# Kernel tuning notes

Hardware: AMD Instinct MI355X
Metric: run time of the kernel (lower is better)

The kernel has to match this reference:

```python
import jax, jax.numpy as jnp
import numpy as np

HEADS = 8
DIM_HEAD = 64
NB_FEATURES = 256
CHUNK = 128          # chunk size used by performer's causal_linear_attention_noncuda
EPS_KERNEL = 1e-4    # eps in softmax_kernel feature map
EPS_DENOM = 1e-6     # eps added to k_cumsum in the denominator


def softmax_kernel(data, proj, is_query):
    # FAVOR+ positive softmax random features (performer_pytorch.softmax_kernel)
    # data: [B,H,N,D], proj: [M,D]
    d = data.shape[-1]
    normalizer = d ** -0.25
    ratio = proj.shape[0] ** -0.5
    data_dash = jnp.einsum('bhnd,md->bhnm', data * normalizer, proj)
    # ||x||^2 / (2*sqrt(d))
    diag = jnp.sum(data * data, axis=-1, keepdims=True) * 0.5 * (normalizer ** 2)
    if is_query:
        m = jax.lax.stop_gradient(jnp.max(data_dash, axis=-1, keepdims=True))
    else:
        m = jax.lax.stop_gradient(jnp.max(data_dash, axis=(-1, -2), keepdims=True))
    return ratio * (jnp.exp(data_dash - diag - m) + EPS_KERNEL)


def causal_linear_attention(qp, kp, v, chunk=CHUNK):
    # Chunked causal linear attention (O(N) in seq len):
    # out_i = q'_i . S_i / (q'_i . z_i), S_i = sum_{j<=i} k'_j v_j^T, z_i = cumsum k'_j
    B, H, N, M = qp.shape
    E = v.shape[-1]
    C = N // chunk

    def to_chunks(x):
        return x.reshape(B, H, C, chunk, x.shape[-1]).transpose(2, 0, 1, 3, 4)

    qc, kc, vc = to_chunks(qp), to_chunks(kp), to_chunks(v)
    k0 = jnp.zeros((B, H, M), qp.dtype)
    s0 = jnp.zeros((B, H, M, E), qp.dtype)

    def step(carry, inp):
        k_last, s_last = carry
        q, k, vv = inp  # [B,H,c,M], [B,H,c,M], [B,H,c,E]
        k_cum = k_last[:, :, None, :] + jnp.cumsum(k, axis=2)           # [B,H,c,M]
        d_inv = 1.0 / jnp.einsum('bhnm,bhnm->bhn', q, k_cum + EPS_DENOM)
        ctx = jnp.einsum('bhnm,bhne->bhnme', k, vv)                      # [B,H,c,M,E]
        s_cum = s_last[:, :, None] + jnp.cumsum(ctx, axis=2)             # [B,H,c,M,E]
        out = jnp.einsum('bhnme,bhnm,bhn->bhne', s_cum, q, d_inv)        # [B,H,c,E]
        return (k_cum[:, :, -1, :], s_cum[:, :, -1]), out

    _, outs = jax.lax.scan(step, (k0, s0), (qc, kc, vc))  # [C,B,H,c,E]
    return outs.transpose(1, 2, 0, 3, 4).reshape(B, H, N, E)


def setup_inputs() -> dict:
    key = jax.random.key(0)
    k1, k2, k3, k4 = jax.random.split(key, 4)
    B, N, D = 4, 2048, 512
    return {
        'query': jax.random.normal(k1, (B, N, D), jnp.float32),
        'key': jax.random.normal(k2, (B, N, D), jnp.float32),
        'value': jax.random.normal(k3, (B, N, D), jnp.float32),
        'projection': jax.random.normal(k4, (NB_FEATURES, DIM_HEAD), jnp.float32),
    }


def reference(query, key, value, projection):
    B, N, D = query.shape

    def split(x):  # [B,N,D] -> [B,H,N,Dh]
        return x.reshape(B, N, HEADS, DIM_HEAD).transpose(0, 2, 1, 3)

    q, k, v = split(query), split(key), split(value)
    qp = softmax_kernel(q, projection, is_query=True)
    kp = softmax_kernel(k, projection, is_query=False)
    out = causal_linear_attention(qp, kp, v)
    return out.transpose(0, 2, 1, 3).reshape(B, N, D)
```

## Files before the change

### kernel.cpp

```cpp
#include <hip/hip_runtime.h>
#include <math.h>

#define BB 4
#define NN 2048
#define DD 512
#define HH 8
#define DH 64
#define MM 256
#define BH 32
#define CHK 128
#define NCH 16
#define ROWS (BH*NN)

constexpr float NRM   = 0.35355339059327373f;
constexpr float RATIO = 0.0625f;
constexpr float EPSK  = 1e-4f;
constexpr float EPSD  = 1e-6f;
constexpr float REPS  = 0.0625f * 1e-4f;

#define OFFB_QP   ((size_t)0)
#define OFFB_SP   ((size_t)33554432)
#define OFFB_KP   (OFFB_SP + (size_t)16777216)
#define OFFB_VT   (OFFB_KP + (size_t)33554432)
#define OFFB_Z    (OFFB_VT + (size_t)8388608)
#define OFFB_KMP  (OFFB_Z  + (size_t)524288)
#define OFFB_SF   (OFFB_KMP + (size_t)4096)
#define OFFB_PJB  (OFFB_SF + (size_t)4096)

typedef __attribute__((ext_vector_type(8))) short short8;
typedef __attribute__((ext_vector_type(4))) float f32x4;

__device__ __forceinline__ float b2f(ushort u) {
  union { float f; unsigned int i; } x; x.i = ((unsigned int)u) << 16; return x.f;
}
__device__ __forceinline__ ushort f2b(float f) {
  unsigned int u = __float_as_uint(f);
  unsigned int r = (u + 0x7FFFu + ((u >> 16) & 1u)) >> 16;
  return (ushort)r;
}

#define MFMA(a,b,c) __builtin_amdgcn_mfma_f32_16x16x32_bf16(a, b, c, 0, 0, 0)

__global__ __launch_bounds__(256) void prep_kernel(const float* __restrict__ proj,
                                                   char* __restrict__ ws) {
  const int i = blockIdx.x*256 + threadIdx.x;
  float4 v = *(const float4*)(proj + (size_t)i*4);
  ushort4 o;
  o.x = f2b(v.x); o.y = f2b(v.y); o.z = f2b(v.z); o.w = f2b(v.w);
  *(ushort4*)((ushort*)(ws + OFFB_PJB) + (size_t)i*4) = o;
}

template<int MODE>
__device__ __forceinline__ void featm_body(const float* __restrict__ inp,
                                           const ushort* __restrict__ projb,
                                           char* __restrict__ ws,
                                           char* lds, int blk) {
  ushort* xh = (ushort*)lds;
  ushort* xl = xh + 64*72;
  ushort* ps = xl + 64*72;
  ushort* qt = (ushort*)lds;
  float* diag_s = (float*)(lds + 36864);
  float (*wmax)[4] = (float(*)[4])(lds + 37120);
  float* kred = (float*)(lds + 38144);

  const int t  = threadIdx.x;
  const int w  = t >> 6;
  const int l  = t & 63;
  const int lq = l >> 4;
  const int ln = l & 15;

  const int rowbase = blk * 64;
  const int bh = rowbase >> 11;
  const int b  = bh >> 3, h = bh & 7;
  const int n0 = rowbase & (NN - 1);

  {
    const int r  = t >> 2;
    const int c0 = (t & 3) * 16;
    const float* src = inp + ((size_t)(b*NN + n0 + r))*DD + h*DH + c0;
    float vv[16];
    #pragma unroll
    for (int j = 0; j < 4; ++j) {
      float4 v = *(const float4*)(src + j*4);
      vv[4*j+0] = v.x*NRM; vv[4*j+1] = v.y*NRM;
      vv[4*j+2] = v.z*NRM; vv[4*j+3] = v.w*NRM;
    }
    float s = 0.f;
    ushort hi[16], lo[16];
    #pragma unroll
    for (int j = 0; j < 16; ++j) {
      s += vv[j]*vv[j];
      hi[j] = f2b(vv[j]);
      lo[j] = f2b(vv[j] - b2f(hi[j]));
    }
    *(short8*)(xh + r*72 + c0)     = *(short8*)&hi[0];
    *(short8*)(xh + r*72 + c0 + 8) = *(short8*)&hi[8];
    *(short8*)(xl + r*72 + c0)     = *(short8*)&lo[0];
    *(short8*)(xl + r*72 + c0 + 8) = *(short8*)&lo[8];
    s += __shfl_xor(s, 1); s += __shfl_xor(s, 2);
    if ((t & 3) == 0) diag_s[r] = 0.5f * s;
  }

  f32x4 acc[4][4];
  #pragma unroll
  for (int mt = 0; mt < 4; ++mt)
    #pragma unroll
    for (int c = 0; c < 4; ++c) acc[mt][c] = (f32x4){0.f,0.f,0.f,0.f};

  #pragma unroll
  for (int p = 0; p < 2; ++p) {
    if (p) __syncthreads();
    #pragma unroll
    for (int ld = 0; ld < 4; ++ld) {
      int flat = t + 256*ld;
      int r = flat >> 3, g = flat & 7;
      *(short8*)(ps + r*72 + g*8) = *(const short8*)(projb + (size_t)(p*128 + r)*DH + g*8);
    }
    __syncthreads();
    #pragma unroll
    for (int kk = 0; kk < 2; ++kk) {
      short8 ah[4], al[4];
      #pragma unroll
      for (int mt = 0; mt < 4; ++mt) {
        ah[mt] = *(const short8*)(xh + (mt*16 + ln)*72 + kk*32 + lq*8);
        al[mt] = *(const short8*)(xl + (mt*16 + ln)*72 + kk*32 + lq*8);
      }
      #pragma unroll
      for (int ntl = 0; ntl < 2; ++ntl) {
        short8 bf = *(const short8*)(ps + (w*32 + ntl*16 + ln)*72 + kk*32 + lq*8);
        #pragma unroll
        for (int mt = 0; mt < 4; ++mt) {
          acc[mt][2*p+ntl] = MFMA(al[mt], bf, acc[mt][2*p+ntl]);
          acc[mt][2*p+ntl] = MFMA(ah[mt], bf, acc[mt][2*p+ntl]);
        }
      }
    }
  }

  if (MODE == 0) {
    #pragma unroll
    for (int mt = 0; mt < 4; ++mt)
      #pragma unroll
      for (int reg = 0; reg < 4; ++reg) {
        float m = acc[mt][0][reg];
        #pragma unroll
        for (int c = 1; c < 4; ++c) m = fmaxf(m, acc[mt][c][reg]);
        m = fmaxf(m, __shfl_xor(m, 1));
        m = fmaxf(m, __shfl_xor(m, 2));
        m = fmaxf(m, __shfl_xor(m, 4));
        m = fmaxf(m, __shfl_xor(m, 8));
        if (ln == 0) wmax[mt*16 + lq*4 + reg][w] = m;
      }
  } else {
    float mx = -1e30f;
    #pragma unroll
    for (int mt = 0; mt < 4; ++mt)
      #pragma unroll
      for (int c = 0; c < 4; ++c)
        #pragma unroll
        for (int reg = 0; reg < 4; ++reg) mx = fmaxf(mx, acc[mt][c][reg]);
    #pragma unroll
    for (int m = 1; m < 64; m <<= 1) mx = fmaxf(mx, __shfl_xor(mx, m));
    if (l == 0) kred[w] = mx;
  }
  __syncthreads();

  float km = 0.f;
  if (MODE == 1) {
    km = fmaxf(fmaxf(kred[0], kred[1]), fmaxf(kred[2], kred[3]));
    if (t == 0) ((float*)(ws + OFFB_KMP))[blk] = km;
  }

  #pragma unroll
  for (int mt = 0; mt < 4; ++mt)
    #pragma unroll
    for (int reg = 0; reg < 4; ++reg) {
      const int row = mt*16 + lq*4 + reg;
      float rm;
      if (MODE == 0) {
        float4 wm4 = *(const float4*)&wmax[row][0];
        rm = fmaxf(fmaxf(wm4.x, wm4.y), fmaxf(wm4.z, wm4.w));
      } else {
        rm = km;
      }
      const float dg = diag_s[row];
      #pragma unroll
      for (int c = 0; c < 4; ++c) {
        const int f = (c >> 1)*128 + w*32 + (c & 1)*16 + ln;
        const float e = __expf(acc[mt][c][reg] - dg - rm);
        qt[row*264 + f] = f2b(MODE == 0 ? RATIO*(e + EPSK) : e);
      }
    }
  __syncthreads();

  ushort* dstbase = (ushort*)(ws + (MODE == 0 ? OFFB_QP : OFFB_KP)) + (size_t)rowbase*MM;
  #pragma unroll
  for (int ld = 0; ld < 8; ++ld) {
    int flat = t + 256*ld;
    int row = flat >> 5, g = flat & 31;
    *(short8*)(dstbase + (size_t)row*MM + g*8) = *(const short8*)(qt + row*264 + g*8);
  }
}

__device__ __forceinline__ void vt_body(const float* __restrict__ value,
                                        char* __restrict__ ws,
                                        char* lds, int blk) {
  float (*vsh)[68] = (float(*)[68])lds;
  const int t = threadIdx.x;
  const int bh = blk >> 4, nc = blk & 15;
  const int b = bh >> 3, h = bh & 7;
  const int n0 = nc * CHK;
  #pragma unroll
  for (int l = 0; l < 8; ++l) {
    int flat = t + 256*l;
    int r = flat >> 4, g = flat & 15;
    *(float4*)&vsh[r][g*4] = *(const float4*)(value + ((size_t)(b*NN + n0 + r))*DD + h*DH + g*4);
  }
  __syncthreads();
  const int e = t & 63, qd = t >> 6;
  ushort* vt = (ushort*)(ws + OFFB_VT) + ((size_t)bh*DH + e)*NN + n0 + qd*32;
  #pragma unroll
  for (int p = 0; p < 16; ++p) {
    unsigned int lo = f2b(vsh[qd*32 + 2*p][e]);
    unsigned int hi = f2b(vsh[qd*32 + 2*p + 1][e]);
    ((unsigned int*)vt)[p] = lo | (hi << 16);
  }
}

__global__ __launch_bounds__(256) void mega_kernel(const float* __restrict__ q,
                                                   const float* __restrict__ k,
                                                   const float* __restrict__ v,
                                                   char* __restrict__ ws) {
  __shared__ __align__(16) char lds[38160];
  const ushort* projb = (const ushort*)(ws + OFFB_PJB);
  const int blk = blockIdx.x;
  if (blk < 1024)       featm_body<0>(q, projb, ws, lds, blk);
  else if (blk < 2048)  featm_body<1>(k, projb, ws, lds, blk - 1024);
  else                  vt_body(v, ws, lds, blk - 2048);
}

__global__ __launch_bounds__(256) void sfac_kernel(char* __restrict__ ws) {
  const int blk = blockIdx.x*256 + threadIdx.x;
  const int bh = blk >> 5;
  const float* kmp = (const float*)(ws + OFFB_KMP);
  float km = -1e30f;
  #pragma unroll
  for (int i = 0; i < 32; ++i) km = fmaxf(km, kmp[bh*32 + i]);
  ((float*)(ws + OFFB_SF))[blk] = RATIO * __expf(kmp[blk] - km);
}

__global__ __launch_bounds__(256) void sprefix_kernel(char* __restrict__ ws) {
  __shared__ __align__(16) unsigned int kpTu[16*68];
  __shared__ __align__(16) ushort Vts[64*136];
  __shared__ float zred[16][16];

  const int t  = threadIdx.x;
  const int w  = t >> 6;
  const int l  = t & 63;
  const int lq = l >> 4;
  const int ln = l & 15;
  const int bh = blockIdx.x >> 4;
  const int ms = blockIdx.x & 15;

  const ushort* kpb = (const ushort*)(ws + OFFB_KP) + (size_t)bh*NN*MM + ms*16;
  const ushort* vtb = (const ushort*)(ws + OFFB_VT) + (size_t)bh*DH*NN;
  const float*  sf  = (const float*)(ws + OFFB_SF);
  ushort* spb = (ushort*)(ws + OFFB_SP) + (size_t)bh*NCH*DH*MM + ms*16;
  float*  zb  = (float*)(ws + OFFB_Z) + (size_t)bh*NCH*MM + ms*16;

  f32x4 acc = (f32x4){0.f,0.f,0.f,0.f};
  float zrun = 0.f;

  for (int tc = 0; tc < NCH; ++tc) {
    __syncthreads();

    if (t < 16) {
      if (tc > 0) {
        float s = 0.f;
        #pragma unroll
        for (int q = 0; q < 16; ++q) s += zred[q][t];
        zrun += s;
      }
      zb[(size_t)tc*MM + t] = zrun;
    }
    {
      ushort* sp = spb + (size_t)tc*DH*MM;
      #pragma unroll
      for (int reg = 0; reg < 4; ++reg)
        sp[(size_t)(w*16 + lq*4 + reg)*MM + ln] = f2b(acc[reg]);
    }

    const ushort* kslice = kpb + (size_t)tc*CHK*MM;
    if (t < 128) {
      int jp = t >> 1, mo = t & 1;
      float s0 = sf[bh*32 + tc*2 + (jp >> 5)];
      short8 a = *(const short8*)(kslice + (size_t)(2*jp)*MM + mo*8);
      short8 c = *(const short8*)(kslice + (size_t)(2*jp+1)*MM + mo*8);
      #pragma unroll
      for (int i = 0; i < 8; ++i) {
        ushort ua = f2b(fmaf(b2f((ushort)a[i]), s0, REPS));
        ushort uc = f2b(fmaf(b2f((ushort)c[i]), s0, REPS));
        kpTu[(mo*8 + i)*68 + jp] = (unsigned int)ua | ((unsigned int)uc << 16);
      }
    }
    #pragma unroll
    for (int it = 0; it < 4; ++it) {
      int slot = t + 256*it;
      int e = slot >> 4, g = slot & 15;
      *(short8*)(Vts + e*136 + g*8) = *(const short8*)(vtb + (size_t)e*NN + tc*CHK + g*8);
    }
    __syncthreads();

    {
      int m = t & 15, q = t >> 4;
      float s = 0.f;
      #pragma unroll
      for (int u = 0; u < 4; ++u) {
        unsigned int p = kpTu[m*68 + q*4 + u];
        s += b2f((ushort)(p & 0xFFFF)) + b2f((ushort)(p >> 16));
      }
      zred[q][m] = s;
    }

    #pragma unroll
    for (int kk = 0; kk < 4; ++kk) {
      short8 af = *(const short8*)(Vts + (w*16 + ln)*136 + kk*32 + lq*8);
      short8 bf = *(const short8*)((const ushort*)kpTu + (size_t)ln*136 + kk*32 + lq*8);
      acc = MFMA(af, bf, acc);
    }
  }
}

__global__ __launch_bounds__(256) void fused_kernel(float* __restrict__ out,
                                                    char* __restrict__ ws) {
  __shared__ __align__(16) char lds[52224];
  __shared__ float den_i[128];
  __shared__ float dinv_s[128];

  const int t  = threadIdx.x;
  const int w  = t >> 6;
  const int l  = t & 63;
  const int lq = l >> 4;
  const int ln = l & 15;
  const int rt0 = w;
  const int rt1 = 7 - w;
  const int blk = blockIdx.x;
  const int bh = blk >> 4, tc = blk & 15;
  const int b = bh >> 3, h = bh & 7;
  const size_t rowbase = (size_t)bh*NN + tc*CHK;

  const ushort* qpg = (const ushort*)(ws + OFFB_QP) + rowbase*MM;
  const ushort* kpg = (const ushort*)(ws + OFFB_KP) + rowbase*MM;
  const ushort* spg = (const ushort*)(ws + OFFB_SP) + (size_t)blk*DH*MM;
  const float*  sf  = (const float*)(ws + OFFB_SF);
  const float sc0 = sf[blk*2], sc1 = sf[blk*2 + 1];

  ushort* qs = (ushort*)lds;
  ushort* ks = qs + 128*72;
  ushort* ss = ks + 128*72;

  f32x4 acc[2][8];
  #pragma unroll
  for (int mt = 0; mt < 2; ++mt)
    #pragma unroll
    for (int nt = 0; nt < 8; ++nt) acc[mt][nt] = (f32x4){0.f,0.f,0.f,0.f};
  f32x4 oacc[2][4];
  #pragma unroll
  for (int mt = 0; mt < 2; ++mt)
    #pragma unroll
    for (int nt = 0; nt < 4; ++nt) oacc[mt][nt] = (f32x4){0.f,0.f,0.f,0.f};

  for (int mc = 0; mc < 4; ++mc) {
    __syncthreads();
    #pragma unroll
    for (int ld2 = 0; ld2 < 4; ++ld2) {
      int flat = t + 256*ld2; int r = flat >> 3, g = flat & 7;
      *(short8*)(qs + r*72 + g*8) = *(const short8*)(qpg + (size_t)r*MM + mc*64 + g*8);
    }
    #pragma unroll
    for (int ld2 = 0; ld2 < 4; ++ld2) {
      int flat = t + 256*ld2; int r = flat >> 3, g = flat & 7;
      short8 kv = *(const short8*)(kpg + (size_t)r*MM + mc*64 + g*8);
      const float sc = (r & 64) ? sc1 : sc0;
      ushort ov[8];
      #pragma unroll
      for (int i = 0; i < 8; ++i) ov[i] = f2b(fmaf(b2f((ushort)kv[i]), sc, REPS));
      *(short8*)(ks + r*72 + g*8) = *(short8*)&ov[0];
    }
    #pragma unroll
    for (int ld2 = 0; ld2 < 2; ++ld2) {
      int flat = t + 256*ld2; int e = flat >> 3, g = flat & 7;
      *(short8*)(ss + e*72 + g*8) = *(const short8*)(spg + (size_t)e*MM + mc*64 + g*8);
    }
    __syncthreads();
    #pragma unroll
    for (int kk = 0; kk < 2; ++kk) {
      short8 af0 = *(const short8*)(qs + (rt0*16 + ln)*72 + kk*32 + lq*8);
      short8 af1 = *(const short8*)(qs + (rt1*16 + ln)*72 + kk*32 + lq*8);
      #pragma unroll
      for (int nt = 0; nt < 8; ++nt) {
        if (nt <= rt1) {
          short8 bf = *(const short8*)(ks + (nt*16 + ln)*72 + kk*32 + lq*8);
          if (nt <= rt0) acc[0][nt] = MFMA(af0, bf, acc[0][nt]);
          acc[1][nt] = MFMA(af1, bf, acc[1][nt]);
        }
      }
      #pragma unroll
      for (int nt = 0; nt < 4; ++nt) {
        short8 bf = *(const short8*)(ss + (nt*16 + ln)*72 + kk*32 + lq*8);
        oacc[0][nt] = MFMA(af0, bf, oacc[0][nt]);
        oacc[1][nt] = MFMA(af1, bf, oacc[1][nt]);
      }
    }
  }

  __syncthreads();

  ushort* P   = (ushort*)lds;
  ushort* Vts = (ushort*)(lds + 34816);

  float rs[2][4] = {{0,0,0,0},{0,0,0,0}};
  #pragma unroll
  for (int mt = 0; mt < 2; ++mt) {
    const int ibase = (mt ? rt1 : rt0) * 16;
    #pragma unroll
    for (int nt = 0; nt < 8; ++nt)
      #pragma unroll
      for (int reg = 0; reg < 4; ++reg) {
        int i = ibase + lq*4 + reg;
        int j = nt*16 + ln;
        float v = (j <= i) ? acc[mt][nt][reg] : 0.f;
        rs[mt][reg] += v;
        P[i*136 + j] = f2b(v);
      }
  }
  #pragma unroll
  for (int mt = 0; mt < 2; ++mt) {
    const int ibase = (mt ? rt1 : rt0) * 16;
    #pragma unroll
    for (int reg = 0; reg < 4; ++reg) {
      float s = rs[mt][reg];
      s += __shfl_xor(s, 1); s += __shfl_xor(s, 2);
      s += __shfl_xor(s, 4); s += __shfl_xor(s, 8);
      if (ln == 0) den_i[ibase + lq*4 + reg] = s;
    }
  }

  const ushort* vtg = (const ushort*)(ws + OFFB_VT) + (size_t)bh*DH*NN + tc*CHK;
  #pragma unroll
  for (int ld2 = 0; ld2 < 4; ++ld2) {
    int flat = t + 256*ld2; int e = flat >> 4, g = flat & 15;
    *(short8*)(Vts + e*136 + g*8) = *(const short8*)(vtg + (size_t)e*NN + g*8);
  }
  __syncthreads();

  {
    const float* zp = (const float*)(ws + OFFB_Z) + (size_t)blk*MM;
    const int r = t >> 1, hf = t & 1;
    const ushort* qrow = qpg + (size_t)r*MM + hf*128;
    float s = 0.f;
    #pragma unroll
    for (int g = 0; g < 16; ++g) {
      short8 qv = *(const short8*)(qrow + g*8);
      const float* zz = zp + hf*128 + g*8;
      #pragma unroll
      for (int x = 0; x < 8; ++x)
        s += b2f((ushort)qv[x]) * (zz[x] + EPSD);
    }
    s += __shfl_xor(s, 1);
    if (hf == 0) dinv_s[r] = 1.0f / (s + den_i[r]);
  }
  __syncthreads();

  #pragma unroll
  for (int kk = 0; kk < 4; ++kk) {
    short8 af0 = *(const short8*)(P + (rt0*16 + ln)*136 + kk*32 + lq*8);
    short8 af1 = *(const short8*)(P + (rt1*16 + ln)*136 + kk*32 + lq*8);
    #pragma unroll
    for (int nt = 0; nt < 4; ++nt) {
      short8 bf = *(const short8*)(Vts + (nt*16 + ln)*136 + kk*32 + lq*8);
      oacc[0][nt] = MFMA(af0, bf, oacc[0][nt]);
      oacc[1][nt] = MFMA(af1, bf, oacc[1][nt]);
    }
  }

  #pragma unroll
  for (int mt = 0; mt < 2; ++mt) {
    const int ibase = (mt ? rt1 : rt0) * 16;
    #pragma unroll
    for (int reg = 0; reg < 4; ++reg) {
      const int i = ibase + lq*4 + reg;
      const float di = dinv_s[i];
      float* dst = out + ((size_t)(b*NN) + tc*CHK + i)*DD + h*DH;
      #pragma unroll
      for (int nt = 0; nt < 4; ++nt)
        dst[nt*16 + ln] = oacc[mt][nt][reg] * di;
    }
  }
}

extern "C" void kernel_launch(void* const* d_in, const int* in_sizes, int n_in,
                              void* d_out, int out_size, void* d_ws, size_t ws_size,
                              hipStream_t stream) {
  (void)in_sizes; (void)n_in; (void)out_size; (void)ws_size;
  const float* q    = (const float*)d_in[0];
  const float* k    = (const float*)d_in[1];
  const float* v    = (const float*)d_in[2];
  const float* proj = (const float*)d_in[3];
  float* out = (float*)d_out;
  char*  ws  = (char*)d_ws;

  prep_kernel<<<16, 256, 0, stream>>>(proj, ws);
  mega_kernel<<<2560, 256, 0, stream>>>(q, k, v, ws);
  sfac_kernel<<<4, 256, 0, stream>>>(ws);
  sprefix_kernel<<<512, 256, 0, stream>>>(ws);
  fused_kernel<<<512, 256, 0, stream>>>(out, ws);
}
```

Before: 188.8 us.

## Fold key scale into sprefix, double-buffer its loads, write scaled kp back

Removes the separate sfac kernel: sprefix now computes the per-head key max and scale factor inline. It also prefetches the next chunk of kp and V into registers with double-buffered LDS, which removes one barrier per iteration. The scaled bf16 kp is written back to the workspace, so fused_kernel loads it directly instead of rescaling. Block-to-head mapping is also permuted, likely for cache locality. This saves a kernel launch and duplicate scaling work, at the cost of an extra global write of kp.

```diff
diff --git a/kernel.cpp b/kernel.cpp
--- a/kernel.cpp
+++ b/kernel.cpp
@@ -239,46 +239,93 @@
   else                  vt_body(v, ws, lds, blk - 2048);
 }
 
-__global__ __launch_bounds__(256) void sfac_kernel(char* __restrict__ ws) {
-  const int blk = blockIdx.x*256 + threadIdx.x;
-  const int bh = blk >> 5;
-  const float* kmp = (const float*)(ws + OFFB_KMP);
-  float km = -1e30f;
-  #pragma unroll
-  for (int i = 0; i < 32; ++i) km = fmaxf(km, kmp[bh*32 + i]);
-  ((float*)(ws + OFFB_SF))[blk] = RATIO * __expf(kmp[blk] - km);
-}
-
 __global__ __launch_bounds__(256) void sprefix_kernel(char* __restrict__ ws) {
-  __shared__ __align__(16) unsigned int kpTu[16*68];
-  __shared__ __align__(16) ushort Vts[64*136];
-  __shared__ float zred[16][16];
+  __shared__ __align__(16) unsigned int kpTu[2][16*68];
+  __shared__ __align__(16) ushort Vts[2][64*136];
+  __shared__ float zred[2][16][16];
 
   const int t  = threadIdx.x;
   const int w  = t >> 6;
   const int l  = t & 63;
   const int lq = l >> 4;
   const int ln = l & 15;
-  const int bh = blockIdx.x >> 4;
-  const int ms = blockIdx.x & 15;
+  const int n  = blockIdx.x;
+  const int k8 = n >> 3;
+  const int bh = (n & 7) + 8*(k8 >> 4);
+  const int ms = k8 & 15;
 
   const ushort* kpb = (const ushort*)(ws + OFFB_KP) + (size_t)bh*NN*MM + ms*16;
+  ushort*       kpw = (ushort*)(ws + OFFB_KP) + (size_t)bh*NN*MM + ms*16;
   const ushort* vtb = (const ushort*)(ws + OFFB_VT) + (size_t)bh*DH*NN;
-  const float*  sf  = (const float*)(ws + OFFB_SF);
   ushort* spb = (ushort*)(ws + OFFB_SP) + (size_t)bh*NCH*DH*MM + ms*16;
   float*  zb  = (float*)(ws + OFFB_Z) + (size_t)bh*NCH*MM + ms*16;
 
+  const float* kmp = (const float*)(ws + OFFB_KMP) + bh*32;
+  float km = kmp[0];
+  #pragma unroll
+  for (int i = 1; i < 32; ++i) km = fmaxf(km, kmp[i]);
+
+  const int jp = t >> 1, mo = t & 1;
+  const int ve = t >> 4, vg = t & 15;
+
+  short8 ka, kc, vr0, vr1, vr2, vr3;
+  if (t < 128) {
+    ka = *(const short8*)(kpb + (size_t)(2*jp)*MM + mo*8);
+    kc = *(const short8*)(kpb + (size_t)(2*jp+1)*MM + mo*8);
+  }
+  vr0 = *(const short8*)(vtb + (size_t)(ve     )*NN + vg*8);
+  vr1 = *(const short8*)(vtb + (size_t)(ve + 16)*NN + vg*8);
+  vr2 = *(const short8*)(vtb + (size_t)(ve + 32)*NN + vg*8);
+  vr3 = *(const short8*)(vtb + (size_t)(ve + 48)*NN + vg*8);
+
   f32x4 acc = (f32x4){0.f,0.f,0.f,0.f};
   float zrun = 0.f;
 
   for (int tc = 0; tc < NCH; ++tc) {
+    const int cur = tc & 1;
+
+    if (t < 128) {
+      const float s0 = RATIO * __expf(kmp[tc*2 + w] - km);
+      ushort ua[8], uc[8];
+      #pragma unroll
+      for (int i = 0; i < 8; ++i) {
+        ua[i] = f2b(fmaf(b2f((ushort)ka[i]), s0, REPS));
+        uc[i] = f2b(fmaf(b2f((ushort)kc[i]), s0, REPS));
+      }
+      #pragma unroll
+      for (int i = 0; i < 8; ++i)
+        kpTu[cur][(mo*8 + i)*68 + jp] = (unsigned int)ua[i] | ((unsigned int)uc[i] << 16);
+      ushort* kwr = kpw + (size_t)tc*CHK*MM + (size_t)(2*jp)*MM + mo*8;
+      *(short8*)kwr        = *(short8*)&ua[0];
+      *(short8*)(kwr + MM) = *(short8*)&uc[0];
+    }
+    {
+      ushort* vb = &Vts[cur][0];
+      *(short8*)(vb + (ve     )*136 + vg*8) = vr0;
+      *(short8*)(vb + (ve + 16)*136 + vg*8) = vr1;
+      *(short8*)(vb + (ve + 32)*136 + vg*8) = vr2;
+      *(short8*)(vb + (ve + 48)*136 + vg*8) = vr3;
+    }
     __syncthreads();
+
+    if (tc + 1 < NCH) {
+      const ushort* ksn = kpb + (size_t)(tc+1)*CHK*MM;
+      if (t < 128) {
+        ka = *(const short8*)(ksn + (size_t)(2*jp)*MM + mo*8);
+        kc = *(const short8*)(ksn + (size_t)(2*jp+1)*MM + mo*8);
+      }
+      const ushort* vtn = vtb + (size_t)(tc+1)*CHK;
+      vr0 = *(const short8*)(vtn + (size_t)(ve     )*NN + vg*8);
+      vr1 = *(const short8*)(vtn + (size_t)(ve + 16)*NN + vg*8);
+      vr2 = *(const short8*)(vtn + (size_t)(ve + 32)*NN + vg*8);
+      vr3 = *(const short8*)(vtn + (size_t)(ve + 48)*NN + vg*8);
+    }
 
     if (t < 16) {
       if (tc > 0) {
         float s = 0.f;
         #pragma unroll
-        for (int q = 0; q < 16; ++q) s += zred[q][t];
+        for (int q = 0; q < 16; ++q) s += zred[cur^1][q][t];
         zrun += s;
       }
       zb[(size_t)tc*MM + t] = zrun;
@@ -289,43 +336,22 @@
       for (int reg = 0; reg < 4; ++reg)
         sp[(size_t)(w*16 + lq*4 + reg)*MM + ln] = f2b(acc[reg]);
     }
-
-    const ushort* kslice = kpb + (size_t)tc*CHK*MM;
-    if (t < 128) {
-      int jp = t >> 1, mo = t & 1;
-      float s0 = sf[bh*32 + tc*2 + (jp >> 5)];
-      short8 a = *(const short8*)(kslice + (size_t)(2*jp)*MM + mo*8);
-      short8 c = *(const short8*)(kslice + (size_t)(2*jp+1)*MM + mo*8);
-      #pragma unroll
-      for (int i = 0; i < 8; ++i) {
-        ushort ua = f2b(fmaf(b2f((ushort)a[i]), s0, REPS));
-        ushort uc = f2b(fmaf(b2f((ushort)c[i]), s0, REPS));
-        kpTu[(mo*8 + i)*68 + jp] = (unsigned int)ua | ((unsigned int)uc << 16);
-      }
-    }
-    #pragma unroll
-    for (int it = 0; it < 4; ++it) {
-      int slot = t + 256*it;
-      int e = slot >> 4, g = slot & 15;
-      *(short8*)(Vts + e*136 + g*8) = *(const short8*)(vtb + (size_t)e*NN + tc*CHK + g*8);
-    }
-    __syncthreads();
 
     {
       int m = t & 15, q = t >> 4;
       float s = 0.f;
       #pragma unroll
       for (int u = 0; u < 4; ++u) {
-        unsigned int p = kpTu[m*68 + q*4 + u];
+        unsigned int p = kpTu[cur][m*68 + q*4 + u];
         s += b2f((ushort)(p & 0xFFFF)) + b2f((ushort)(p >> 16));
       }
-      zred[q][m] = s;
+      zred[cur][q][m] = s;
     }
 
     #pragma unroll
     for (int kk = 0; kk < 4; ++kk) {
-      short8 af = *(const short8*)(Vts + (w*16 + ln)*136 + kk*32 + lq*8);
-      short8 bf = *(const short8*)((const ushort*)kpTu + (size_t)ln*136 + kk*32 + lq*8);
+      short8 af = *(const short8*)(&Vts[cur][0] + (w*16 + ln)*136 + kk*32 + lq*8);
+      short8 bf = *(const short8*)((const ushort*)&kpTu[cur][0] + (size_t)ln*136 + kk*32 + lq*8);
       acc = MFMA(af, bf, acc);
     }
   }
@@ -352,8 +378,6 @@
   const ushort* qpg = (const ushort*)(ws + OFFB_QP) + rowbase*MM;
   const ushort* kpg = (const ushort*)(ws + OFFB_KP) + rowbase*MM;
   const ushort* spg = (const ushort*)(ws + OFFB_SP) + (size_t)blk*DH*MM;
-  const float*  sf  = (const float*)(ws + OFFB_SF);
-  const float sc0 = sf[blk*2], sc1 = sf[blk*2 + 1];
 
   ushort* qs = (ushort*)lds;
   ushort* ks = qs + 128*72;
@@ -380,12 +404,7 @@
     #pragma unroll
     for (int ld2 = 0; ld2 < 4; ++ld2) {
       int flat = t + 256*ld2; int r = flat >> 3, g = flat & 7;
-      short8 kv = *(const short8*)(kpg + (size_t)r*MM + mc*64 + g*8);
-      const float sc = (r & 64) ? sc1 : sc0;
-      ushort ov[8];
-      #pragma unroll
-      for (int i = 0; i < 8; ++i) ov[i] = f2b(fmaf(b2f((ushort)kv[i]), sc, REPS));
-      *(short8*)(ks + r*72 + g*8) = *(short8*)&ov[0];
+      *(short8*)(ks + r*72 + g*8) = *(const short8*)(kpg + (size_t)r*MM + mc*64 + g*8);
     }
     #pragma unroll
     for (int ld2 = 0; ld2 < 2; ++ld2) {
@@ -512,7 +531,6 @@
 
   prep_kernel<<<16, 256, 0, stream>>>(proj, ws);
   mega_kernel<<<2560, 256, 0, stream>>>(q, k, v, ws);
-  sfac_kernel<<<4, 256, 0, stream>>>(ws);
   sprefix_kernel<<<512, 256, 0, stream>>>(ws);
   fused_kernel<<<512, 256, 0, stream>>>(out, ws);
 }
```

After: 182.4 us. 3.4% less time.
